# Performance work log

Hardware: AMD Instinct MI355X
Metric: run time of the kernel (lower is better)

The kernel has to match this reference:

```python
import jax, jax.numpy as jnp
import numpy as np
from jax import lax

B, C, H, W = 8, 128, 256, 256
Q = 3            # polynomial order of SuperONN2d
K = 3            # kernel size
OC = C // 2      # SuperONN2d out channels
EPS = 1e-5       # LayerNorm eps (torch default)


def setup_inputs() -> dict:
    key = jax.random.key(0)
    k1, k2, k3 = jax.random.split(key, 3)
    x = jax.random.normal(k1, (B, C, H, W), dtype=jnp.float32)
    gamma = jnp.ones((C,), dtype=jnp.float32)
    beta = jnp.zeros((C,), dtype=jnp.float32)
    # SuperONN2d weight: (out_ch, q*in_ch, k, k), bias=False
    fan_in = Q * C * K * K
    Wc = jax.random.uniform(k2, (OC, Q * C, K, K), dtype=jnp.float32,
                            minval=-1.0, maxval=1.0) / np.sqrt(fan_in)
    return {"x": x, "gamma": gamma, "beta": beta, "Wc": Wc}


def _pixel_unshuffle2(y):
    # torch.nn.PixelUnshuffle(2): (B,C,H,W) -> (B,4C,H/2,W/2)
    b, c, h, w = y.shape
    y = y.reshape(b, c, h // 2, 2, w // 2, 2)
    y = y.transpose(0, 1, 3, 5, 2, 4)
    return y.reshape(b, c * 4, h // 2, w // 2)


def reference(x, gamma, beta, Wc):
    # LayerNormNLP2d: normalize over channel dim at each pixel
    mu = jnp.mean(x, axis=1, keepdims=True)
    var = jnp.mean(jnp.square(x - mu), axis=1, keepdims=True)
    xn = (x - mu) * lax.rsqrt(var + EPS)
    xn = xn * gamma[None, :, None, None] + beta[None, :, None, None]
    # SuperONN2d: concat powers x^1..x^Q on channels, then a single conv (no bias)
    xp = jnp.concatenate([xn ** (i + 1) for i in range(Q)], axis=1)  # (B, Q*C, H, W)
    y = lax.conv_general_dilated(
        xp, Wc, window_strides=(1, 1), padding=[(K // 2, K // 2)] * 2,
        dimension_numbers=("NCHW", "OIHW", "NCHW"))                  # (B, OC, H, W)
    return _pixel_unshuffle2(y)                                       # (B, 2C, H/2, W/2)
```

## Files before the change

### kernel.cpp

```cpp
#include <hip/hip_runtime.h>
#include <hip/hip_bf16.h>
#include <stdint.h>

#define BB   8
#define CCH  128
#define HH   256
#define WWD  256
#define OCC  64
#define HWW  (HH*WWD)
#define PLANE (BB*HWW*32)
#define PITCH 208

typedef __attribute__((ext_vector_type(8))) short  bf16x8;
typedef __attribute__((ext_vector_type(4))) float  f32x4;
typedef __attribute__((ext_vector_type(4))) unsigned int u32x4;
typedef __attribute__((ext_vector_type(2))) float  f32x2;

static __device__ __forceinline__ unsigned cvt_pk_bf16(float lo, float hi) {
    unsigned r;
    asm("v_cvt_pk_bf16_f32 %0, %1, %2" : "=v"(r) : "v"(lo), "v"(hi));
    return r;
}
static __device__ __forceinline__ float bf16lo_to_f(unsigned u) {
    union { unsigned u; float f; } c; c.u = u << 16; return c.f;
}
static __device__ __forceinline__ float bf16hi_to_f(unsigned u) {
    union { unsigned u; float f; } c; c.u = u & 0xffff0000u; return c.f;
}

__global__ void prep_w(const float* __restrict__ Wc, unsigned short* __restrict__ Wb2) {
    int task = blockIdx.x * 256 + threadIdx.x;
    int lane = task & 63;
    int frag = task >> 6;
    int nt   = frag & 3;
    int cc   = (frag >> 2) & 3;
    int tq   = frag >> 4;
    int q    = tq % 3;
    int tap  = tq / 3;
    int oc   = nt * 16 + (lane & 15);
    int kb   = cc * 32 + (lane >> 4) * 8;
    u32x4 o;
    #pragma unroll
    for (int k = 0; k < 4; ++k) {
        float v0 = Wc[(size_t)(oc * 384 + q * 128 + kb + 2 * k) * 9 + tap];
        float v1 = Wc[(size_t)(oc * 384 + q * 128 + kb + 2 * k + 1) * 9 + tap];
        o[k] = cvt_pk_bf16(v0, v1);
    }
    *(u32x4*)(Wb2 + (size_t)task * 8) = o;
}

__global__ __launch_bounds__(256) void ln_kernel(
        const float* __restrict__ x, const float* __restrict__ gamma,
        const float* __restrict__ beta, unsigned short* __restrict__ xn2) {
    int p  = blockIdx.x * 256 + threadIdx.x;
    int b  = p >> 16;
    int hw = p & 65535;
    const float* xb = x + (size_t)b * CCH * HWW + hw;
    unsigned buf[64];
    float sum = 0.f, sumsq = 0.f;
    #pragma unroll
    for (int cp = 0; cp < 64; ++cp) {
        float v0 = xb[(size_t)(2 * cp) * HWW];
        float v1 = xb[(size_t)(2 * cp + 1) * HWW];
        sum   += v0 + v1;
        sumsq += v0 * v0 + v1 * v1;
        buf[cp] = cvt_pk_bf16(v0, v1);
    }
    float mu  = sum * (1.f / 128.f);
    float var = sumsq * (1.f / 128.f) - mu * mu;
    float rs  = rsqrtf(var + 1e-5f);
    size_t pix = (size_t)p * 32;
    #pragma unroll
    for (int g = 0; g < 16; ++g) {
        u32x4 o;
        #pragma unroll
        for (int k = 0; k < 4; ++k) {
            int cp = g * 4 + k;
            float f0 = bf16lo_to_f(buf[cp]);
            float f1 = bf16hi_to_f(buf[cp]);
            int c0 = cp * 2, c1 = cp * 2 + 1;
            float y0 = fmaf((f0 - mu) * rs, gamma[c0], beta[c0]);
            float y1 = fmaf((f1 - mu) * rs, gamma[c1], beta[c1]);
            o[k] = cvt_pk_bf16(y0, y1);
        }
        *(u32x4*)(xn2 + (size_t)(g >> 2) * PLANE + pix + (g & 3) * 8) = o;
    }
}

__global__ __launch_bounds__(256, 2) void conv_kernel(
        const unsigned short* __restrict__ xn2,
        const unsigned short* __restrict__ Wb2,
        float* __restrict__ out) {
    __shared__ __align__(16) unsigned char P[10 * 34 * PITCH];

    int bid = blockIdx.x;
    int bx  = bid & 7;
    int by  = (bid >> 3) & 31;
    int b   = bid >> 8;
    int x0  = bx * 32;
    int y0  = by * 8;
    int tid  = threadIdx.x;
    int lane = tid & 63;
    int w    = tid >> 6;
    int l15  = lane & 15;
    int l4   = lane >> 4;

    f32x4 acc[4][4];
    #pragma unroll
    for (int mt = 0; mt < 4; ++mt)
        #pragma unroll
        for (int nt = 0; nt < 4; ++nt)
            acc[mt][nt] = (f32x4){0.f, 0.f, 0.f, 0.f};

    int offg[6];
    int woff[6];
    bool vldf[6], wrf[6];
    #pragma unroll
    for (int it = 0; it < 6; ++it) {
        int item = tid + it * 256;
        bool ok  = item < 1360;
        int ii   = ok ? item : 0;
        int row  = ii / 136;
        int rem  = ii - row * 136;
        int px   = rem >> 2;
        int g    = rem & 3;
        int yy   = y0 - 1 + row;
        int xx   = x0 - 1 + px;
        bool inb = ok && (unsigned)yy < 256u && (unsigned)xx < 256u;
        offg[it] = (yy * 256 + xx) * 32 + g * 8;
        woff[it] = (row * 34 + px) * PITCH + g * 16;
        vldf[it] = inb;
        wrf[it]  = ok;
    }

    const unsigned short* xpb = xn2 + (size_t)b * HWW * 32;
    const bf16x8* wlane = (const bf16x8*)Wb2 + lane;
    const unsigned char* pa = P + (2 * w * 34 + l15) * PITCH + l4 * 16;

    u32x4 rs[6];
    #pragma unroll
    for (int it = 0; it < 6; ++it) {
        u32x4 v = (u32x4){0u, 0u, 0u, 0u};
        if (vldf[it]) v = *(const u32x4*)(xpb + offg[it]);
        rs[it] = v;
    }

    #pragma unroll 1
    for (int cc = 0; cc < 4; ++cc) {
        if (cc > 0) __syncthreads();
        #pragma unroll
        for (int it = 0; it < 6; ++it) {
            if (!wrf[it]) continue;
            u32x4 u1 = rs[it];
            u32x4 u2, u3;
            #pragma unroll
            for (int k = 0; k < 4; ++k) {
                float f0 = bf16lo_to_f(u1[k]);
                float f1 = bf16hi_to_f(u1[k]);
                float s0 = f0 * f0, s1 = f1 * f1;
                u2[k] = cvt_pk_bf16(s0, s1);
                u3[k] = cvt_pk_bf16(s0 * f0, s1 * f1);
            }
            unsigned char* cell = P + woff[it];
            *(u32x4*)(cell)       = u1;
            *(u32x4*)(cell + 64)  = u2;
            *(u32x4*)(cell + 128) = u3;
        }
        __syncthreads();

        if (cc < 3) {
            const unsigned short* xpn = xpb + (size_t)(cc + 1) * PLANE;
            #pragma unroll
            for (int it = 0; it < 6; ++it) {
                u32x4 v = (u32x4){0u, 0u, 0u, 0u};
                if (vldf[it]) v = *(const u32x4*)(xpn + offg[it]);
                rs[it] = v;
            }
        }

        const bf16x8* wcc = wlane + cc * 4 * 64;
        bf16x8 av[2][4], bvv[2][4];
        #pragma unroll
        for (int mt = 0; mt < 4; ++mt)
            av[0][mt] = *(const bf16x8*)(pa + ((mt >> 1)) * (34 * PITCH)
                                            + ((mt & 1) * 16) * PITCH);
        #pragma unroll
        for (int nt = 0; nt < 4; ++nt)
            bvv[0][nt] = wcc[nt * 64];

        #pragma unroll
        for (int tq = 0; tq < 27; ++tq) {
            int cur = tq & 1, nxt = cur ^ 1;
            if (tq < 26) {
                int t2 = tq + 1;
                int ky = t2 / 9, kx = (t2 / 3) % 3, q = t2 % 3;
                #pragma unroll
                for (int mt = 0; mt < 4; ++mt)
                    av[nxt][mt] = *(const bf16x8*)(pa
                        + ((mt >> 1) + ky) * (34 * PITCH)
                        + ((mt & 1) * 16 + kx) * PITCH + q * 64);
                #pragma unroll
                for (int nt = 0; nt < 4; ++nt)
                    bvv[nxt][nt] = wcc[(t2 * 16 + nt) * 64];
            }
            __builtin_amdgcn_s_setprio(1);
            #pragma unroll
            for (int nt = 0; nt < 4; ++nt)
                #pragma unroll
                for (int mt = 0; mt < 4; ++mt)
                    acc[mt][nt] = __builtin_amdgcn_mfma_f32_16x16x32_bf16(
                        av[cur][mt], bvv[cur][nt], acc[mt][nt], 0, 0, 0);
            __builtin_amdgcn_s_setprio(0);
        }
    }

    #pragma unroll
    for (int mt = 0; mt < 4; ++mt) {
        int y  = y0 + 2 * w + (mt >> 1);
        int s  = (mt >> 1);
        int y2 = y >> 1;
        int X0 = x0 + (mt & 1) * 16 + l4 * 4;
        int x2 = X0 >> 1;
        #pragma unroll
        for (int nt = 0; nt < 4; ++nt) {
            int oc = nt * 16 + l15;
            #pragma unroll
            for (int rr = 0; rr < 2; ++rr) {
                int ch = oc * 4 + s * 2 + rr;
                size_t off = ((size_t)(b * 256 + ch) * 128 + y2) * 128 + x2;
                f32x2 v;
                v.x = acc[mt][nt][rr];
                v.y = acc[mt][nt][rr + 2];
                *(f32x2*)(out + off) = v;
            }
        }
    }
}

extern "C" void kernel_launch(void* const* d_in, const int* in_sizes, int n_in,
                              void* d_out, int out_size, void* d_ws, size_t ws_size,
                              hipStream_t stream) {
    const float* x     = (const float*)d_in[0];
    const float* gamma = (const float*)d_in[1];
    const float* beta  = (const float*)d_in[2];
    const float* Wc    = (const float*)d_in[3];
    float* out = (float*)d_out;

    const size_t xn_bytes = (size_t)4 * PLANE * 2;
    const size_t wb_bytes = (size_t)27 * 16 * 512 * 2;
    if (ws_size < xn_bytes + wb_bytes) return;
    unsigned short* xn2 = (unsigned short*)d_ws;
    unsigned short* Wb2 = (unsigned short*)((char*)d_ws + xn_bytes);

    hipLaunchKernelGGL(prep_w, dim3(108), dim3(256), 0, stream, Wc, Wb2);
    hipLaunchKernelGGL(ln_kernel, dim3(2048), dim3(256), 0, stream, x, gamma, beta, xn2);
    hipLaunchKernelGGL(conv_kernel, dim3(2048), dim3(256), 0, stream, xn2, Wb2, out);
}
```

Measured before the change: 296.3 us.

## Switch conv MFMA from 16x16x32 to 32x32x16 with repacked weights and LDS layout

Replaces the 16x16x32 bf16 MFMA tiling (4x4 fragments per wave) with 32x32x16 MFMAs (2x2 fragments, split K halves). It repacks the weights for the new operand layout and restructures the LDS tile into a planar channel-group layout with 16-byte cells. The epilogue is rewritten to match the 32x32 accumulator layout. The goal is fewer MFMA issues and fewer operand loads per FLOP, at the cost of a different LDS access pattern that may cause bank conflicts.

Measured after the change: 326.1 us. 1.1x slower.

```diff
diff --git a/kernel.cpp b/kernel.cpp
--- a/kernel.cpp
+++ b/kernel.cpp
@@ -9,12 +9,11 @@
 #define OCC  64
 #define HWW  (HH*WWD)
 #define PLANE (BB*HWW*32)
-#define PITCH 208
-
-typedef __attribute__((ext_vector_type(8))) short  bf16x8;
-typedef __attribute__((ext_vector_type(4))) float  f32x4;
-typedef __attribute__((ext_vector_type(4))) unsigned int u32x4;
-typedef __attribute__((ext_vector_type(2))) float  f32x2;
+
+typedef __attribute__((ext_vector_type(8)))  short  bf16x8;
+typedef __attribute__((ext_vector_type(16))) float  f32x16;
+typedef __attribute__((ext_vector_type(4)))  unsigned int u32x4;
+typedef __attribute__((ext_vector_type(2)))  float  f32x2;
 
 static __device__ __forceinline__ unsigned cvt_pk_bf16(float lo, float hi) {
     unsigned r;
@@ -28,17 +27,18 @@
     union { unsigned u; float f; } c; c.u = u & 0xffff0000u; return c.f;
 }
 
-__global__ void prep_w(const float* __restrict__ Wc, unsigned short* __restrict__ Wb2) {
-    int task = blockIdx.x * 256 + threadIdx.x;
-    int lane = task & 63;
-    int frag = task >> 6;
-    int nt   = frag & 3;
-    int cc   = (frag >> 2) & 3;
-    int tq   = frag >> 4;
+__global__ void prep_w(const float* __restrict__ Wc, unsigned short* __restrict__ Wb3) {
+    int t = blockIdx.x * 256 + threadIdx.x;
+    int lane = t & 63;
+    int f    = t >> 6;
+    int nt   = f & 1;
+    int kh   = (f >> 1) & 1;
+    int cc   = (f >> 2) & 3;
+    int tq   = f >> 4;
     int q    = tq % 3;
     int tap  = tq / 3;
-    int oc   = nt * 16 + (lane & 15);
-    int kb   = cc * 32 + (lane >> 4) * 8;
+    int oc   = nt * 32 + (lane & 31);
+    int kb   = cc * 32 + kh * 16 + (lane >> 5) * 8;
     u32x4 o;
     #pragma unroll
     for (int k = 0; k < 4; ++k) {
@@ -46,7 +46,7 @@
         float v1 = Wc[(size_t)(oc * 384 + q * 128 + kb + 2 * k + 1) * 9 + tap];
         o[k] = cvt_pk_bf16(v0, v1);
     }
-    *(u32x4*)(Wb2 + (size_t)task * 8) = o;
+    *(u32x4*)(Wb3 + (size_t)t * 8) = o;
 }
 
 __global__ __launch_bounds__(256) void ln_kernel(
@@ -89,9 +89,9 @@
 
 __global__ __launch_bounds__(256, 2) void conv_kernel(
         const unsigned short* __restrict__ xn2,
-        const unsigned short* __restrict__ Wb2,
+        const unsigned short* __restrict__ Wb3,
         float* __restrict__ out) {
-    __shared__ __align__(16) unsigned char P[10 * 34 * PITCH];
+    __shared__ __align__(16) unsigned char P[10 * 12 * 34 * 16];
 
     int bid = blockIdx.x;
     int bx  = bid & 7;
@@ -102,15 +102,17 @@
     int tid  = threadIdx.x;
     int lane = tid & 63;
     int w    = tid >> 6;
-    int l15  = lane & 15;
-    int l4   = lane >> 4;
-
-    f32x4 acc[4][4];
-    #pragma unroll
-    for (int mt = 0; mt < 4; ++mt)
-        #pragma unroll
-        for (int nt = 0; nt < 4; ++nt)
-            acc[mt][nt] = (f32x4){0.f, 0.f, 0.f, 0.f};
+    int l31  = lane & 31;
+    int kb   = lane >> 5;
+
+    f32x16 acc[2][2];
+    #pragma unroll
+    for (int mt = 0; mt < 2; ++mt)
+        #pragma unroll
+        for (int nt = 0; nt < 2; ++nt)
+            #pragma unroll
+            for (int r = 0; r < 16; ++r)
+                acc[mt][nt][r] = 0.f;
 
     int offg[6];
     int woff[6];
@@ -123,19 +125,19 @@
         int row  = ii / 136;
         int rem  = ii - row * 136;
         int px   = rem >> 2;
-        int g    = rem & 3;
+        int g2   = rem & 3;
         int yy   = y0 - 1 + row;
         int xx   = x0 - 1 + px;
         bool inb = ok && (unsigned)yy < 256u && (unsigned)xx < 256u;
-        offg[it] = (yy * 256 + xx) * 32 + g * 8;
-        woff[it] = (row * 34 + px) * PITCH + g * 16;
+        offg[it] = (yy * 256 + xx) * 32 + g2 * 8;
+        woff[it] = (row * 12 + g2) * 34 + px;
         vldf[it] = inb;
         wrf[it]  = ok;
     }
 
     const unsigned short* xpb = xn2 + (size_t)b * HWW * 32;
-    const bf16x8* wlane = (const bf16x8*)Wb2 + lane;
-    const unsigned char* pa = P + (2 * w * 34 + l15) * PITCH + l4 * 16;
+    const bf16x8* wlane = (const bf16x8*)Wb3 + lane;
+    const unsigned char* pa = P + ((size_t)kb * 34 + l31) * 16;
 
     u32x4 rs[6];
     #pragma unroll
@@ -161,10 +163,10 @@
                 u2[k] = cvt_pk_bf16(s0, s1);
                 u3[k] = cvt_pk_bf16(s0 * f0, s1 * f1);
             }
-            unsigned char* cell = P + woff[it];
-            *(u32x4*)(cell)       = u1;
-            *(u32x4*)(cell + 64)  = u2;
-            *(u32x4*)(cell + 128) = u3;
+            unsigned char* cell = P + (size_t)woff[it] * 16;
+            *(u32x4*)(cell)            = u1;
+            *(u32x4*)(cell + 4*34*16)  = u2;
+            *(u32x4*)(cell + 8*34*16)  = u3;
         }
         __syncthreads();
 
@@ -178,59 +180,71 @@
             }
         }
 
-        const bf16x8* wcc = wlane + cc * 4 * 64;
-        bf16x8 av[2][4], bvv[2][4];
-        #pragma unroll
-        for (int mt = 0; mt < 4; ++mt)
-            av[0][mt] = *(const bf16x8*)(pa + ((mt >> 1)) * (34 * PITCH)
-                                            + ((mt & 1) * 16) * PITCH);
-        #pragma unroll
-        for (int nt = 0; nt < 4; ++nt)
-            bvv[0][nt] = wcc[nt * 64];
+        const bf16x8* wcc = wlane + (size_t)cc * 4 * 64;
+        bf16x8 av[2][2][2], bv[2][2][2];
+        #pragma unroll
+        for (int mt = 0; mt < 2; ++mt)
+            #pragma unroll
+            for (int kh = 0; kh < 2; ++kh)
+                av[0][mt][kh] = *(const bf16x8*)(pa
+                    + (size_t)(((2 * w + mt) * 12 + kh * 2) * 34) * 16);
+        #pragma unroll
+        for (int nt = 0; nt < 2; ++nt)
+            #pragma unroll
+            for (int kh = 0; kh < 2; ++kh)
+                bv[0][nt][kh] = wcc[(kh * 2 + nt) * 64];
 
         #pragma unroll
         for (int tq = 0; tq < 27; ++tq) {
-            int cur = tq & 1, nxt = cur ^ 1;
+            const int cur = tq & 1, nxt = cur ^ 1;
             if (tq < 26) {
-                int t2 = tq + 1;
-                int ky = t2 / 9, kx = (t2 / 3) % 3, q = t2 % 3;
+                const int t2 = tq + 1;
+                const int ky = t2 / 9, kx = (t2 / 3) % 3, q = t2 % 3;
                 #pragma unroll
-                for (int mt = 0; mt < 4; ++mt)
-                    av[nxt][mt] = *(const bf16x8*)(pa
-                        + ((mt >> 1) + ky) * (34 * PITCH)
-                        + ((mt & 1) * 16 + kx) * PITCH + q * 64);
+                for (int mt = 0; mt < 2; ++mt)
+                    #pragma unroll
+                    for (int kh = 0; kh < 2; ++kh)
+                        av[nxt][mt][kh] = *(const bf16x8*)(pa
+                            + (size_t)((((2 * w + mt + ky) * 12 + q * 4 + kh * 2) * 34)
+                                       + kx) * 16);
                 #pragma unroll
-                for (int nt = 0; nt < 4; ++nt)
-                    bvv[nxt][nt] = wcc[(t2 * 16 + nt) * 64];
+                for (int nt = 0; nt < 2; ++nt)
+                    #pragma unroll
+                    for (int kh = 0; kh < 2; ++kh)
+                        bv[nxt][nt][kh] = wcc[((size_t)t2 * 16 + kh * 2 + nt) * 64];
             }
             __builtin_amdgcn_s_setprio(1);
             #pragma unroll
-            for (int nt = 0; nt < 4; ++nt)
+            for (int kh = 0; kh < 2; ++kh)
                 #pragma unroll
-                for (int mt = 0; mt < 4; ++mt)
-                    acc[mt][nt] = __builtin_amdgcn_mfma_f32_16x16x32_bf16(
-                        av[cur][mt], bvv[cur][nt], acc[mt][nt], 0, 0, 0);
+                for (int nt = 0; nt < 2; ++nt)
+                    #pragma unroll
+                    for (int mt = 0; mt < 2; ++mt)
+                        acc[mt][nt] = __builtin_amdgcn_mfma_f32_32x32x16_bf16(
+                            av[cur][mt][kh], bv[cur][nt][kh], acc[mt][nt], 0, 0, 0);
             __builtin_amdgcn_s_setprio(0);
         }
     }
 
     #pragma unroll
-    for (int mt = 0; mt < 4; ++mt) {
-        int y  = y0 + 2 * w + (mt >> 1);
-        int s  = (mt >> 1);
+    for (int mt = 0; mt < 2; ++mt) {
+        int y  = y0 + 2 * w + mt;
+        int s  = mt;
         int y2 = y >> 1;
-        int X0 = x0 + (mt & 1) * 16 + l4 * 4;
-        int x2 = X0 >> 1;
-        #pragma unroll
-        for (int nt = 0; nt < 4; ++nt) {
-            int oc = nt * 16 + l15;
-            #pragma unroll
-            for (int rr = 0; rr < 2; ++rr) {
-                int ch = oc * 4 + s * 2 + rr;
+        #pragma unroll
+        for (int nt = 0; nt < 2; ++nt) {
+            int oc = nt * 32 + l31;
+            #pragma unroll
+            for (int p = 0; p < 8; ++p) {
+                const int r  = (p & 1) + (p >> 1) * 4;
+                int px = (r & 3) + 8 * (r >> 2) + 4 * kb;
+                int x  = x0 + px;
+                int ch = oc * 4 + s * 2 + (x & 1);
+                int x2 = x >> 1;
                 size_t off = ((size_t)(b * 256 + ch) * 128 + y2) * 128 + x2;
                 f32x2 v;
-                v.x = acc[mt][nt][rr];
-                v.y = acc[mt][nt][rr + 2];
+                v.x = acc[mt][nt][r];
+                v.y = acc[mt][nt][r + 2];
                 *(f32x2*)(out + off) = v;
             }
         }
@@ -247,12 +261,12 @@
     float* out = (float*)d_out;
 
     const size_t xn_bytes = (size_t)4 * PLANE * 2;
-    const size_t wb_bytes = (size_t)27 * 16 * 512 * 2;
+    const size_t wb_bytes = (size_t)27648 * 16;
     if (ws_size < xn_bytes + wb_bytes) return;
     unsigned short* xn2 = (unsigned short*)d_ws;
-    unsigned short* Wb2 = (unsigned short*)((char*)d_ws + xn_bytes);
-
-    hipLaunchKernelGGL(prep_w, dim3(108), dim3(256), 0, stream, Wc, Wb2);
+    unsigned short* Wb3 = (unsigned short*)((char*)d_ws + xn_bytes);
+
+    hipLaunchKernelGGL(prep_w, dim3(108), dim3(256), 0, stream, Wc, Wb3);
     hipLaunchKernelGGL(ln_kernel, dim3(2048), dim3(256), 0, stream, x, gamma, beta, xn2);
-    hipLaunchKernelGGL(conv_kernel, dim3(2048), dim3(256), 0, stream, xn2, Wb2, out);
-}
+    hipLaunchKernelGGL(conv_kernel, dim3(2048), dim3(256), 0, stream, xn2, Wb3, out);
+}
```
